# Performance work log

Measured on AMD Instinct MI355X. Metric: run time of the kernel, lower is better.

Reference implementation:

```python
import jax, jax.numpy as jnp
import numpy as np

DN = ('NHWC', 'HWIO', 'NHWC')
EPS = 1e-3  # Keras BatchNormalization default epsilon


def conv2d(x, w):
    return jax.lax.conv_general_dilated(x, w, (1, 1), 'SAME', dimension_numbers=DN)


def hard_sigmoid(x):
    # Keras ConvLSTM2D default recurrent_activation
    return jnp.clip(0.2 * x + 0.5, 0.0, 1.0)


def convlstm2d(x, Wx, Wh, b):
    """Keras ConvLSTM2D, return_sequences=True. x: (B,T,H,W,C).
    Wx: (3,3,C,4F) input kernel, Wh: (3,3,F,4F) recurrent kernel, b: (4F,).
    Gate order (Keras): i, f, c, o."""
    B, T, H, W, C = x.shape
    F = Wh.shape[2]
    # input-to-gate convs for all timesteps in one batched conv
    xg = conv2d(x.reshape(B * T, H, W, C), Wx) + b          # (B*T,H,W,4F)
    xg = xg.reshape(B, T, H, W, 4 * F).transpose(1, 0, 2, 3, 4)  # (T,B,H,W,4F)

    def step(carry, xg_t):
        h, c = carry
        g = xg_t + conv2d(h, Wh)                            # (B,H,W,4F)
        i, f, cc, o = jnp.split(g, 4, axis=-1)
        i = hard_sigmoid(i)
        f = hard_sigmoid(f)
        o = hard_sigmoid(o)
        c = f * c + i * jnp.tanh(cc)
        h = o * jnp.tanh(c)
        return (h, c), h

    h0 = jnp.zeros((B, H, W, F), x.dtype)
    (_, _), hs = jax.lax.scan(step, (h0, h0), xg)           # hs: (T,B,H,W,F)
    return hs.transpose(1, 0, 2, 3, 4)


def batchnorm(x, gamma, beta):
    # training-mode BN over all axes except channel (last)
    mu = x.mean(axis=(0, 1, 2, 3), keepdims=True)
    var = x.var(axis=(0, 1, 2, 3), keepdims=True)
    return gamma * (x - mu) * jax.lax.rsqrt(var + EPS) + beta


def setup_inputs() -> dict:
    key = jax.random.key(0)
    B, T, H, W, C = 4, 8, 16, 16, 256
    F = 256
    ks = jax.random.split(key, 10)
    s = 0.02
    inp = {
        'input_tensor': jax.random.normal(ks[0], (B, T, H, W, C), jnp.float32),
        'Wx1': jax.random.normal(ks[1], (3, 3, C, 4 * F), jnp.float32) * s,
        'Wh1': jax.random.normal(ks[2], (3, 3, F, 4 * F), jnp.float32) * s,
        'b1': jnp.zeros((4 * F,), jnp.float32),
        'g1': jnp.ones((F,), jnp.float32),
        'be1': jnp.zeros((F,), jnp.float32),
        'Wx2': jax.random.normal(ks[3], (3, 3, F, 4 * F), jnp.float32) * s,
        'Wh2': jax.random.normal(ks[4], (3, 3, F, 4 * F), jnp.float32) * s,
        'b2': jnp.zeros((4 * F,), jnp.float32),
        'g2': jnp.ones((F,), jnp.float32),
        'be2': jnp.zeros((F,), jnp.float32),
        'Wx3': jax.random.normal(ks[5], (3, 3, F, 4 * F), jnp.float32) * s,
        'Wh3': jax.random.normal(ks[6], (3, 3, F, 4 * F), jnp.float32) * s,
        'b3': jnp.zeros((4 * F,), jnp.float32),
        'g3': jnp.ones((F,), jnp.float32),
        'be3': jnp.zeros((F,), jnp.float32),
    }
    return inp


def reference(input_tensor, Wx1, Wh1, b1, g1, be1,
              Wx2, Wh2, b2, g2, be2,
              Wx3, Wh3, b3, g3, be3):
    x = batchnorm(convlstm2d(input_tensor, Wx1, Wh1, b1), g1, be1)
    x = batchnorm(convlstm2d(x, Wx2, Wh2, b2), g2, be2)
    x = batchnorm(convlstm2d(x, Wx3, Wh3, b3), g3, be3)
    return x
```

## Files before the change

kernel.cpp:

```cpp
#include <hip/hip_runtime.h>

#define HW      256
#define COUT    1024
#define TSTEPS  8
#define BN_EPS  1e-3f
#define KTOT    2304

typedef unsigned short u16;
typedef unsigned int   u32;
typedef __attribute__((ext_vector_type(8))) _Float16 v8h;
typedef __attribute__((ext_vector_type(4))) float v4f;

__device__ __forceinline__ u16 f2h(float x) {
    _Float16 h = (_Float16)x; return *(u16*)&h;
}
__device__ __forceinline__ float h2f(u16 u) {
    _Float16 h = *(_Float16*)&u; return (float)h;
}
__device__ __forceinline__ float hsig(float x) {
    return fminf(fmaxf(0.2f * x + 0.5f, 0.f), 1.f);
}

typedef __attribute__((address_space(1))) const unsigned int gas_u32;
typedef __attribute__((address_space(3))) unsigned int las_u32;
__device__ __forceinline__ void gl16(const void* g, void* l) {
    __builtin_amdgcn_global_load_lds((gas_u32*)g, (las_u32*)l, 16, 0, 0);
}

__global__ __launch_bounds__(256, 2) void conv_big_k(
    const u16* __restrict__ apad,
    const u16* __restrict__ wT,
    const float* __restrict__ bias,
    u16* __restrict__ out)
{
    constexpr int KQ = 36;
    __shared__ u16 lds[2 * 16384];

    const int bid = blockIdx.x;
    const int xcd = bid & 7, idx = bid >> 3;
    const int by = (xcd >> 1) * 2 + (idx & 1);
    const int bx = (xcd & 1) * 32 + (idx >> 1);
    const int m0 = bx * 128, n0 = by * 128;
    const int tid = threadIdx.x, lane = tid & 63, w = tid >> 6;
    const int wr = w >> 1, wc = w & 1;
    const int lr = lane >> 3;
    const int g  = (lane & 7) ^ lr;
    const int fr = lane & 15, kc = lane >> 4;

    const char* a_src[4];
    #pragma unroll
    for (int i = 0; i < 4; ++i) {
        int m = m0 + w * 32 + i * 8 + lr;
        int img = m >> 8, pix = m & 255, yy = pix >> 4, xx = pix & 15;
        a_src[i] = (const char*)apad + ((((long)img * 18 + yy) * 18 + xx) * 256 + g * 8) * 2;
    }
    const char* b_src[4];
    #pragma unroll
    for (int i = 0; i < 4; ++i) {
        int n = n0 + w * 32 + i * 8 + lr;
        b_src[i] = (const char*)wT + ((long)n * KTOT + g * 8) * 2;
    }

    int aro[4][2], bro[4][2];
    #pragma unroll
    for (int mi = 0; mi < 4; ++mi) {
        int rl = wr * 64 + mi * 16 + fr;
        #pragma unroll
        for (int ks = 0; ks < 2; ++ks)
            aro[mi][ks] = rl * 128 + ((((ks << 2) | kc) ^ (fr & 7)) << 4);
    }
    #pragma unroll
    for (int ni = 0; ni < 4; ++ni) {
        int nr = wc * 64 + ni * 16 + fr;
        #pragma unroll
        for (int ks = 0; ks < 2; ++ks)
            bro[ni][ks] = 16384 + nr * 128 + ((((ks << 2) | kc) ^ (fr & 7)) << 4);
    }

    v4f acc[4][4];
    #pragma unroll
    for (int mi = 0; mi < 4; ++mi)
        #pragma unroll
        for (int ni = 0; ni < 4; ++ni) acc[mi][ni] = (v4f)0.f;

#define STAGE_B(J) { int j_ = (J); int dxy = j_ >> 2, c64 = j_ & 3;           \
    int dy = (dxy * 11) >> 5; int dx = dxy - dy * 3;                          \
    int aoff = ((dy * 18 + dx) * 256 + c64 * 64) * 2; int boff = j_ * 128;    \
    char* base = (char*)lds + (j_ & 1) * 32768;                               \
    _Pragma("unroll") for (int i = 0; i < 4; ++i)                             \
        gl16(a_src[i] + aoff, base + (w * 32 + i * 8) * 128);                 \
    _Pragma("unroll") for (int i = 0; i < 4; ++i)                             \
        gl16(b_src[i] + boff, base + 16384 + (w * 32 + i * 8) * 128); }

#define COMPUTE_B(J) { const char* base = (const char*)lds + ((J) & 1) * 32768; \
    v8h af[4][2], bf[4][2];                                                   \
    _Pragma("unroll") for (int mi = 0; mi < 4; ++mi)                          \
        _Pragma("unroll") for (int ks = 0; ks < 2; ++ks)                      \
            af[mi][ks] = *(const v8h*)(base + aro[mi][ks]);                   \
    _Pragma("unroll") for (int ni = 0; ni < 4; ++ni)                          \
        _Pragma("unroll") for (int ks = 0; ks < 2; ++ks)                      \
            bf[ni][ks] = *(const v8h*)(base + bro[ni][ks]);                   \
    __builtin_amdgcn_s_setprio(1);                                            \
    _Pragma("unroll") for (int ks = 0; ks < 2; ++ks)                          \
    _Pragma("unroll") for (int mi = 0; mi < 4; ++mi)                          \
    _Pragma("unroll") for (int ni = 0; ni < 4; ++ni)                          \
        acc[mi][ni] = __builtin_amdgcn_mfma_f32_16x16x32_f16(af[mi][ks], bf[ni][ks], acc[mi][ni], 0, 0, 0); \
    __builtin_amdgcn_s_setprio(0); }

    STAGE_B(0);
    for (int kq = 0; kq < KQ - 1; ++kq) {
        asm volatile("s_waitcnt vmcnt(0)" ::: "memory");
        __builtin_amdgcn_s_barrier();
        __builtin_amdgcn_sched_barrier(0);
        STAGE_B(kq + 1);
        COMPUTE_B(kq);
    }
    asm volatile("s_waitcnt vmcnt(0)" ::: "memory");
    __builtin_amdgcn_s_barrier();
    __builtin_amdgcn_sched_barrier(0);
    COMPUTE_B(KQ - 1);
#undef STAGE_B
#undef COMPUTE_B

    #pragma unroll
    for (int mi = 0; mi < 4; ++mi) {
        #pragma unroll
        for (int ni = 0; ni < 4; ++ni) {
            int mrow = m0 + wr * 64 + mi * 16 + ((lane >> 4) << 2);
            int ncol = n0 + wc * 64 + ni * 16 + fr;
            float b0 = bias[(ncol & 3) * 256 + (ncol >> 2)];
            #pragma unroll
            for (int r = 0; r < 4; ++r)
                out[(long)(mrow + r) * COUT + ncol] = f2h(acc[mi][ni][r] + b0);
        }
    }
}

__global__ __launch_bounds__(256, 2) void rec_fused_k(
    const u16* __restrict__ ph_in,
    const u16* __restrict__ wT,
    const u16* __restrict__ xg,
    float* __restrict__ cbuf,
    float* __restrict__ hs,
    u16* __restrict__ ph_out,
    int t)
{
    constexpr int KQ = 36;
    __shared__ u16 lds[3 * 6144];

    const int bid = blockIdx.x;
    const int k8 = bid & 7, q = bid >> 3;
    const int by = k8 * 2 + (q >> 5), bx = q & 31;
    const int m0 = bx * 32, n0 = by * 64;
    const int tid = threadIdx.x, lane = tid & 63, wv = tid >> 6;
    const int lr = lane >> 3, g = (lane & 7) ^ lr;
    const int fr = lane & 15, kc = lane >> 4;

    const char* a_src;
    { int m = m0 + wv * 8 + lr;
      int img = m >> 8, pix = m & 255, yy = pix >> 4, xx = pix & 15;
      a_src = (const char*)ph_in + ((((long)img * 18 + yy) * 18 + xx) * 256 + g * 8) * 2; }
    const char* b_src[2];
    #pragma unroll
    for (int i = 0; i < 2; ++i) {
        int n = n0 + wv * 16 + i * 8 + lr;
        b_src[i] = (const char*)wT + ((long)n * KTOT + g * 8) * 2;
    }

    int aro[2][2], bro[2];
    #pragma unroll
    for (int mi = 0; mi < 2; ++mi)
        #pragma unroll
        for (int ks = 0; ks < 2; ++ks)
            aro[mi][ks] = (mi * 16 + fr) * 128 + ((((ks << 2) | kc) ^ (fr & 7)) << 4);
    #pragma unroll
    for (int ks = 0; ks < 2; ++ks)
        bro[ks] = 4096 + (wv * 16 + fr) * 128 + ((((ks << 2) | kc) ^ (fr & 7)) << 4);

    v4f acc0 = (v4f)0.f, acc1 = (v4f)0.f;

#define STAGE_R(J) { int j_ = (J); int dxy = j_ >> 2, c64 = j_ & 3;           \
    int dy = (dxy * 11) >> 5; int dx = dxy - dy * 3;                          \
    int aoff = ((dy * 18 + dx) * 256 + c64 * 64) * 2; int boff = j_ * 128;    \
    char* base = (char*)lds + (j_ % 3) * 12288;                               \
    gl16(a_src + aoff, base + (wv * 8) * 128);                                \
    gl16(b_src[0] + boff, base + 4096 + (wv * 16) * 128);                     \
    gl16(b_src[1] + boff, base + 4096 + (wv * 16 + 8) * 128); }

#define COMPUTE_R(J) { const char* base = (const char*)lds + ((J) % 3) * 12288; \
    v8h a00 = *(const v8h*)(base + aro[0][0]);                                \
    v8h a01 = *(const v8h*)(base + aro[0][1]);                                \
    v8h a10 = *(const v8h*)(base + aro[1][0]);                                \
    v8h a11 = *(const v8h*)(base + aro[1][1]);                                \
    v8h b0  = *(const v8h*)(base + bro[0]);                                   \
    v8h b1  = *(const v8h*)(base + bro[1]);                                   \
    __builtin_amdgcn_s_setprio(1);                                            \
    acc0 = __builtin_amdgcn_mfma_f32_16x16x32_f16(a00, b0, acc0, 0, 0, 0);    \
    acc1 = __builtin_amdgcn_mfma_f32_16x16x32_f16(a10, b0, acc1, 0, 0, 0);    \
    acc0 = __builtin_amdgcn_mfma_f32_16x16x32_f16(a01, b1, acc0, 0, 0, 0);    \
    acc1 = __builtin_amdgcn_mfma_f32_16x16x32_f16(a11, b1, acc1, 0, 0, 0);    \
    __builtin_amdgcn_s_setprio(0); }

    STAGE_R(0); STAGE_R(1);
    for (int kq = 0; kq < KQ - 2; ++kq) {
        asm volatile("s_waitcnt vmcnt(3)" ::: "memory");
        __builtin_amdgcn_s_barrier();
        __builtin_amdgcn_sched_barrier(0);
        STAGE_R(kq + 2);
        COMPUTE_R(kq);
    }
    asm volatile("s_waitcnt vmcnt(3)" ::: "memory");
    __builtin_amdgcn_s_barrier();
    __builtin_amdgcn_sched_barrier(0);
    COMPUTE_R(KQ - 2);
    asm volatile("s_waitcnt vmcnt(0)" ::: "memory");
    __builtin_amdgcn_s_barrier();
    __builtin_amdgcn_sched_barrier(0);
    COMPUTE_R(KQ - 1);
#undef STAGE_R
#undef COMPUTE_R

    v4f accA[2] = {acc0, acc1};
    const bool gl0 = lane & 1, gl1 = lane & 2;
    #pragma unroll
    for (int mi = 0; mi < 2; ++mi) {
        float V0 = accA[mi][0], V1 = accA[mi][1];
        float V2 = accA[mi][2], V3 = accA[mi][3];
        float x0 = __shfl_xor(V0, 1), x1 = __shfl_xor(V1, 1);
        float x2 = __shfl_xor(V2, 1), x3 = __shfl_xor(V3, 1);
        float a0 = gl0 ? x1 : V0;
        float a1 = gl0 ? V1 : x0;
        float a2 = gl0 ? x3 : V2;
        float a3 = gl0 ? V3 : x2;
        float s0 = __shfl_xor(a0, 2), s1 = __shfl_xor(a1, 2);
        float s2 = __shfl_xor(a2, 2), s3 = __shfl_xor(a3, 2);
        float Ti = gl1 ? s2 : a0;
        float Tf = gl1 ? s3 : a1;
        float Tc = gl1 ? a2 : s0;
        float To = gl1 ? a3 : s1;

        int row = m0 + mi * 16 + ((lane >> 4) << 2) + (lane & 3);
        int f4  = n0 + wv * 16 + (lane & 12);
        int img = row >> 8, pix = row & 255, fch = f4 >> 2;
        long xrow = ((long)(img * TSTEPS + t) * HW + pix);
        uint2 xb = *(const uint2*)&xg[xrow * COUT + f4];
        float pi = Ti + h2f((u16)(xb.x & 0xffff));
        float pf = Tf + h2f((u16)(xb.x >> 16));
        float pc = Tc + h2f((u16)(xb.y & 0xffff));
        float po = To + h2f((u16)(xb.y >> 16));
        long cidx = (long)row * 256 + fch;
        float c = hsig(pf) * cbuf[cidx] + hsig(pi) * tanhf(pc);
        float h = hsig(po) * tanhf(c);
        cbuf[cidx] = c;
        hs[xrow * 256 + fch] = h;
        int yy = pix >> 4, xx = pix & 15;
        ph_out[(((long)img * 18 + yy + 1) * 18 + xx + 1) * 256 + fch] = f2h(h);
    }
}

__global__ __launch_bounds__(256) void wprep_k(const float* __restrict__ w,
                                               u16* __restrict__ wT)
{
    int k0 = blockIdx.x * 32;
    int np = blockIdx.y * 256 + threadIdx.x;
    int n  = (np & 3) * 256 + (np >> 2);
    u32 pk[16];
    #pragma unroll
    for (int kk = 0; kk < 32; kk += 2) {
        float a = w[(long)(k0 + kk) * COUT + n];
        float b = w[(long)(k0 + kk + 1) * COUT + n];
        pk[kk >> 1] = (u32)f2h(a) | ((u32)f2h(b) << 16);
    }
    uint4* dst = (uint4*)&wT[(long)np * KTOT + k0];
    dst[0] = make_uint4(pk[0], pk[1], pk[2], pk[3]);
    dst[1] = make_uint4(pk[4], pk[5], pk[6], pk[7]);
    dst[2] = make_uint4(pk[8], pk[9], pk[10], pk[11]);
    dst[3] = make_uint4(pk[12], pk[13], pk[14], pk[15]);
}

__global__ __launch_bounds__(256) void convert_x_k(const float* __restrict__ x,
                                                   u16* __restrict__ padx)
{
    int q = blockIdx.x * 256 + threadIdx.x;
    int e0 = q * 4;
    int f = e0 & 255, pix = (e0 >> 8) & 255, img = e0 >> 16;
    float4 v = ((const float4*)x)[q];
    int yy = pix >> 4, xx = pix & 15;
    long o = (((long)img * 18 + yy + 1) * 18 + xx + 1) * 256 + f;
    u32 lo = (u32)f2h(v.x) | ((u32)f2h(v.y) << 16);
    u32 hi = (u32)f2h(v.z) | ((u32)f2h(v.w) << 16);
    *(uint2*)&padx[o] = make_uint2(lo, hi);
}

__global__ __launch_bounds__(256) void bn_stats1_k(
    const float* __restrict__ x, float* __restrict__ partial)
{
    const int tid = threadIdx.x;
    const int blk = blockIdx.x;
    float s = 0.f, s2 = 0.f;
    const long base = (long)blk * 16 * 256;
    #pragma unroll
    for (int gi = 0; gi < 16; ++gi) {
        float v = x[base + gi * 256 + tid];
        s += v; s2 += v * v;
    }
    partial[blk * 512 + tid]       = s;
    partial[blk * 512 + 256 + tid] = s2;
}

__global__ __launch_bounds__(256) void bn_stats2_k(
    const float* __restrict__ partial, const float* __restrict__ gamma,
    const float* __restrict__ beta, float* __restrict__ stats)
{
    const int f = threadIdx.x;
    float s = 0.f, s2 = 0.f;
    for (int b = 0; b < 512; ++b) {
        s  += partial[b * 512 + f];
        s2 += partial[b * 512 + 256 + f];
    }
    const float inv_n = 1.f / 8192.f;
    float mu  = s * inv_n;
    float var = s2 * inv_n - mu * mu;
    float sc  = gamma[f] * rsqrtf(var + BN_EPS);
    stats[f]       = sc;
    stats[256 + f] = beta[f] - mu * sc;
}

__global__ __launch_bounds__(256) void bn_apply_k(
    const float* __restrict__ x, const float* __restrict__ stats,
    u16* __restrict__ padx, float* __restrict__ out)
{
    const int q = blockIdx.x * 256 + threadIdx.x;
    const int e0 = q * 4;
    const int f = e0 & 255, pix = (e0 >> 8) & 255, img = e0 >> 16;
    float4 v  = ((const float4*)x)[q];
    float4 sc = *(const float4*)(stats + f);
    float4 sh = *(const float4*)(stats + 256 + f);
    v.x = v.x * sc.x + sh.x;
    v.y = v.y * sc.y + sh.y;
    v.z = v.z * sc.z + sh.z;
    v.w = v.w * sc.w + sh.w;
    if (out) ((float4*)out)[q] = v;
    if (padx) {
        int yy = pix >> 4, xx = pix & 15;
        long o = (((long)img * 18 + yy + 1) * 18 + xx + 1) * 256 + f;
        u32 lo = (u32)f2h(v.x) | ((u32)f2h(v.y) << 16);
        u32 hi = (u32)f2h(v.z) | ((u32)f2h(v.w) << 16);
        *(uint2*)&padx[o] = make_uint2(lo, hi);
    }
}

extern "C" void kernel_launch(void* const* d_in, const int* in_sizes, int n_in,
                              void* d_out, int out_size, void* d_ws, size_t ws_size,
                              hipStream_t stream)
{
    const float* x0    = (const float*)d_in[0];
    const float* Wx[3] = {(const float*)d_in[1], (const float*)d_in[6],  (const float*)d_in[11]};
    const float* Wh[3] = {(const float*)d_in[2], (const float*)d_in[7],  (const float*)d_in[12]};
    const float* bb[3] = {(const float*)d_in[3], (const float*)d_in[8],  (const float*)d_in[13]};
    const float* gg[3] = {(const float*)d_in[4], (const float*)d_in[9],  (const float*)d_in[14]};
    const float* be[3] = {(const float*)d_in[5], (const float*)d_in[10], (const float*)d_in[15]};

    float* ws    = (float*)d_ws;
    u16*  xg     = (u16*)ws;
    float* cbuf  = ws   + 4194304;
    float* hs    = cbuf + 262144;
    float* part  = hs   + 2097152;
    float* stats = part + 262144;
    u16*  pad_x  = (u16*)(stats + 512);
    u16*  pad_h  = pad_x + 2654208;
    u16*  wTx    = pad_h + 663552;
    u16*  wTh    = wTx   + 2359296;
    const long PHN = 331776;

    hipMemsetAsync(pad_x, 0, 2654208 * sizeof(u16), stream);
    hipLaunchKernelGGL(convert_x_k, dim3(2048), dim3(256), 0, stream, x0, pad_x);

    for (int l = 0; l < 3; ++l) {
        hipLaunchKernelGGL(wprep_k, dim3(72, 4), dim3(256), 0, stream, Wx[l], wTx);
        hipLaunchKernelGGL(wprep_k, dim3(72, 4), dim3(256), 0, stream, Wh[l], wTh);

        hipLaunchKernelGGL(conv_big_k, dim3(512), dim3(256), 0, stream,
            pad_x, wTx, bb[l], xg);

        hipMemsetAsync(pad_h, 0, 2 * PHN * sizeof(u16), stream);
        hipMemsetAsync(cbuf, 0, 262144 * sizeof(float), stream);

        for (int t = 0; t < TSTEPS; ++t) {
            hipLaunchKernelGGL(rec_fused_k, dim3(512), dim3(256), 0, stream,
                pad_h + (t & 1) * PHN, wTh, xg, cbuf, hs,
                pad_h + ((t & 1) ^ 1) * PHN, t);
        }

        hipLaunchKernelGGL(bn_stats1_k, dim3(512), dim3(256), 0, stream, hs, part);
        hipLaunchKernelGGL(bn_stats2_k, dim3(1), dim3(256), 0, stream, part, gg[l], be[l], stats);
        hipLaunchKernelGGL(bn_apply_k, dim3(2048), dim3(256), 0, stream, hs, stats,
            (l < 2) ? pad_x : (u16*)nullptr, (l == 2) ? (float*)d_out : (float*)nullptr);
    }
}
```

Before: 587.2 us.

## Restructure recurrent GEMM with fragment-ordered weights and skip zero-state first step

The recurrent kernel now uses 64x64 tiles with 256 blocks. Weights are pre-packed into MFMA fragment order by a new prep kernel and loaded straight into registers, double-buffered, instead of being staged through LDS. Timestep 0, where h and c are zero, is replaced by a gate-only kernel, which removes one recurrent GEMM per layer. The padded h buffer is zeroed once rather than per layer, and BN stats use fewer, larger partial blocks. In exchange, 256 blocks on this GPU gives lower occupancy and less latency hiding, and the register-held B fragments raise register pressure.

```diff
diff --git a/kernel.cpp b/kernel.cpp
--- a/kernel.cpp
+++ b/kernel.cpp
@@ -136,94 +136,104 @@
     }
 }
 
-__global__ __launch_bounds__(256, 2) void rec_fused_k(
+__global__ __launch_bounds__(256) void rec_fused_k(
     const u16* __restrict__ ph_in,
-    const u16* __restrict__ wT,
+    const u16* __restrict__ wTf,
     const u16* __restrict__ xg,
     float* __restrict__ cbuf,
     float* __restrict__ hs,
     u16* __restrict__ ph_out,
     int t)
 {
-    constexpr int KQ = 36;
-    __shared__ u16 lds[3 * 6144];
+    __shared__ u16 lds[3 * 4096];
 
     const int bid = blockIdx.x;
-    const int k8 = bid & 7, q = bid >> 3;
-    const int by = k8 * 2 + (q >> 5), bx = q & 31;
-    const int m0 = bx * 32, n0 = by * 64;
-    const int tid = threadIdx.x, lane = tid & 63, wv = tid >> 6;
+    const int by = (bid & 7) * 2 + ((bid >> 3) & 1);
+    const int bx = bid >> 4;
+    const int m0 = bx * 64, n0 = by * 64;
+    const int tid = threadIdx.x, lane = tid & 63, w = tid >> 6;
     const int lr = lane >> 3, g = (lane & 7) ^ lr;
     const int fr = lane & 15, kc = lane >> 4;
 
-    const char* a_src;
-    { int m = m0 + wv * 8 + lr;
-      int img = m >> 8, pix = m & 255, yy = pix >> 4, xx = pix & 15;
-      a_src = (const char*)ph_in + ((((long)img * 18 + yy) * 18 + xx) * 256 + g * 8) * 2; }
-    const char* b_src[2];
+    const char* a_src[2];
     #pragma unroll
     for (int i = 0; i < 2; ++i) {
-        int n = n0 + wv * 16 + i * 8 + lr;
-        b_src[i] = (const char*)wT + ((long)n * KTOT + g * 8) * 2;
-    }
-
-    int aro[2][2], bro[2];
-    #pragma unroll
-    for (int mi = 0; mi < 2; ++mi)
+        int m = m0 + w * 16 + i * 8 + lr;
+        int img = m >> 8, pix = m & 255, yy = pix >> 4, xx = pix & 15;
+        a_src[i] = (const char*)ph_in + ((((long)img * 18 + yy) * 18 + xx) * 256 + g * 8) * 2;
+    }
+    const char* b_base = (const char*)wTf + ((long)(by * 4 + w) * 72) * 1024 + lane * 16;
+
+    int aro[4][2];
+    #pragma unroll
+    for (int mi = 0; mi < 4; ++mi)
         #pragma unroll
         for (int ks = 0; ks < 2; ++ks)
             aro[mi][ks] = (mi * 16 + fr) * 128 + ((((ks << 2) | kc) ^ (fr & 7)) << 4);
-    #pragma unroll
-    for (int ks = 0; ks < 2; ++ks)
-        bro[ks] = 4096 + (wv * 16 + fr) * 128 + ((((ks << 2) | kc) ^ (fr & 7)) << 4);
-
-    v4f acc0 = (v4f)0.f, acc1 = (v4f)0.f;
-
-#define STAGE_R(J) { int j_ = (J); int dxy = j_ >> 2, c64 = j_ & 3;           \
+
+    v4f acc0 = (v4f)0.f, acc1 = (v4f)0.f, acc2 = (v4f)0.f, acc3 = (v4f)0.f;
+    v8h b0x, b0y, b1x, b1y;
+
+#define STAGE_A(J) { int j_ = (J); int dxy = j_ >> 2, c64 = j_ & 3;           \
     int dy = (dxy * 11) >> 5; int dx = dxy - dy * 3;                          \
-    int aoff = ((dy * 18 + dx) * 256 + c64 * 64) * 2; int boff = j_ * 128;    \
-    char* base = (char*)lds + (j_ % 3) * 12288;                               \
-    gl16(a_src + aoff, base + (wv * 8) * 128);                                \
-    gl16(b_src[0] + boff, base + 4096 + (wv * 16) * 128);                     \
-    gl16(b_src[1] + boff, base + 4096 + (wv * 16 + 8) * 128); }
-
-#define COMPUTE_R(J) { const char* base = (const char*)lds + ((J) % 3) * 12288; \
-    v8h a00 = *(const v8h*)(base + aro[0][0]);                                \
-    v8h a01 = *(const v8h*)(base + aro[0][1]);                                \
-    v8h a10 = *(const v8h*)(base + aro[1][0]);                                \
-    v8h a11 = *(const v8h*)(base + aro[1][1]);                                \
-    v8h b0  = *(const v8h*)(base + bro[0]);                                   \
-    v8h b1  = *(const v8h*)(base + bro[1]);                                   \
+    int aoff = ((dy * 18 + dx) * 256 + c64 * 64) * 2;                         \
+    char* dst = (char*)lds + (j_ % 3) * 8192 + (w * 16) * 128;                \
+    gl16(a_src[0] + aoff, dst); gl16(a_src[1] + aoff, dst + 1024); }
+
+#define LDB(J, RX, RY) { RX = *(const v8h*)(b_base + (2 * (J)) * 1024);       \
+                         RY = *(const v8h*)(b_base + (2 * (J) + 1) * 1024); }
+
+#define COMPUTE(J, RX, RY) { const char* base = (const char*)lds + ((J) % 3) * 8192; \
+    v8h af0 = *(const v8h*)(base + aro[0][0]);                                \
+    v8h af1 = *(const v8h*)(base + aro[1][0]);                                \
+    v8h af2 = *(const v8h*)(base + aro[2][0]);                                \
+    v8h af3 = *(const v8h*)(base + aro[3][0]);                                \
+    v8h ag0 = *(const v8h*)(base + aro[0][1]);                                \
+    v8h ag1 = *(const v8h*)(base + aro[1][1]);                                \
+    v8h ag2 = *(const v8h*)(base + aro[2][1]);                                \
+    v8h ag3 = *(const v8h*)(base + aro[3][1]);                                \
     __builtin_amdgcn_s_setprio(1);                                            \
-    acc0 = __builtin_amdgcn_mfma_f32_16x16x32_f16(a00, b0, acc0, 0, 0, 0);    \
-    acc1 = __builtin_amdgcn_mfma_f32_16x16x32_f16(a10, b0, acc1, 0, 0, 0);    \
-    acc0 = __builtin_amdgcn_mfma_f32_16x16x32_f16(a01, b1, acc0, 0, 0, 0);    \
-    acc1 = __builtin_amdgcn_mfma_f32_16x16x32_f16(a11, b1, acc1, 0, 0, 0);    \
+    acc0 = __builtin_amdgcn_mfma_f32_16x16x32_f16(af0, RX, acc0, 0, 0, 0);    \
+    acc1 = __builtin_amdgcn_mfma_f32_16x16x32_f16(af1, RX, acc1, 0, 0, 0);    \
+    acc2 = __builtin_amdgcn_mfma_f32_16x16x32_f16(af2, RX, acc2, 0, 0, 0);    \
+    acc3 = __builtin_amdgcn_mfma_f32_16x16x32_f16(af3, RX, acc3, 0, 0, 0);    \
+    acc0 = __builtin_amdgcn_mfma_f32_16x16x32_f16(ag0, RY, acc0, 0, 0, 0);    \
+    acc1 = __builtin_amdgcn_mfma_f32_16x16x32_f16(ag1, RY, acc1, 0, 0, 0);    \
+    acc2 = __builtin_amdgcn_mfma_f32_16x16x32_f16(ag2, RY, acc2, 0, 0, 0);    \
+    acc3 = __builtin_amdgcn_mfma_f32_16x16x32_f16(ag3, RY, acc3, 0, 0, 0);    \
     __builtin_amdgcn_s_setprio(0); }
 
-    STAGE_R(0); STAGE_R(1);
-    for (int kq = 0; kq < KQ - 2; ++kq) {
-        asm volatile("s_waitcnt vmcnt(3)" ::: "memory");
+    STAGE_A(0); LDB(0, b0x, b0y); STAGE_A(1);
+    for (int j = 0; j < 17; ++j) {
+        int kq = 2 * j;
+        asm volatile("s_waitcnt vmcnt(2)" ::: "memory");
         __builtin_amdgcn_s_barrier();
         __builtin_amdgcn_sched_barrier(0);
-        STAGE_R(kq + 2);
-        COMPUTE_R(kq);
-    }
-    asm volatile("s_waitcnt vmcnt(3)" ::: "memory");
+        LDB(kq + 1, b1x, b1y); STAGE_A(kq + 2);
+        COMPUTE(kq, b0x, b0y);
+        asm volatile("s_waitcnt vmcnt(2)" ::: "memory");
+        __builtin_amdgcn_s_barrier();
+        __builtin_amdgcn_sched_barrier(0);
+        LDB(kq + 2, b0x, b0y); STAGE_A(kq + 3);
+        COMPUTE(kq + 1, b1x, b1y);
+    }
+    asm volatile("s_waitcnt vmcnt(2)" ::: "memory");
     __builtin_amdgcn_s_barrier();
     __builtin_amdgcn_sched_barrier(0);
-    COMPUTE_R(KQ - 2);
+    LDB(35, b1x, b1y);
+    COMPUTE(34, b0x, b0y);
     asm volatile("s_waitcnt vmcnt(0)" ::: "memory");
     __builtin_amdgcn_s_barrier();
     __builtin_amdgcn_sched_barrier(0);
-    COMPUTE_R(KQ - 1);
-#undef STAGE_R
-#undef COMPUTE_R
-
-    v4f accA[2] = {acc0, acc1};
+    COMPUTE(35, b1x, b1y);
+#undef STAGE_A
+#undef LDB
+#undef COMPUTE
+
+    v4f accA[4] = {acc0, acc1, acc2, acc3};
     const bool gl0 = lane & 1, gl1 = lane & 2;
     #pragma unroll
-    for (int mi = 0; mi < 2; ++mi) {
+    for (int mi = 0; mi < 4; ++mi) {
         float V0 = accA[mi][0], V1 = accA[mi][1];
         float V2 = accA[mi][2], V3 = accA[mi][3];
         float x0 = __shfl_xor(V0, 1), x1 = __shfl_xor(V1, 1);
@@ -240,7 +250,7 @@
         float To = gl1 ? a3 : s1;
 
         int row = m0 + mi * 16 + ((lane >> 4) << 2) + (lane & 3);
-        int f4  = n0 + wv * 16 + (lane & 12);
+        int f4  = n0 + w * 16 + (lane & 12);
         int img = row >> 8, pix = row & 255, fch = f4 >> 2;
         long xrow = ((long)(img * TSTEPS + t) * HW + pix);
         uint2 xb = *(const uint2*)&xg[xrow * COUT + f4];
@@ -258,6 +268,26 @@
     }
 }
 
+__global__ __launch_bounds__(256) void gates0_k(
+    const u16* __restrict__ xg, float* __restrict__ cbuf,
+    float* __restrict__ hs, u16* __restrict__ ph_out)
+{
+    int idx = blockIdx.x * 256 + threadIdx.x;
+    int fch = idx & 255, row = idx >> 8;
+    int img = row >> 8, pix = row & 255;
+    long xrow = (long)(img * TSTEPS) * HW + pix;
+    uint2 xb = *(const uint2*)&xg[xrow * COUT + fch * 4];
+    float pi = h2f((u16)(xb.x & 0xffff));
+    float pc = h2f((u16)(xb.y & 0xffff));
+    float po = h2f((u16)(xb.y >> 16));
+    float c = hsig(pi) * tanhf(pc);
+    float h = hsig(po) * tanhf(c);
+    cbuf[(long)row * 256 + fch] = c;
+    hs[xrow * 256 + fch] = h;
+    int yy = pix >> 4, xx = pix & 15;
+    ph_out[(((long)img * 18 + yy + 1) * 18 + xx + 1) * 256 + fch] = f2h(h);
+}
+
 __global__ __launch_bounds__(256) void wprep_k(const float* __restrict__ w,
                                                u16* __restrict__ wT)
 {
@@ -276,6 +306,26 @@
     dst[1] = make_uint4(pk[4], pk[5], pk[6], pk[7]);
     dst[2] = make_uint4(pk[8], pk[9], pk[10], pk[11]);
     dst[3] = make_uint4(pk[12], pk[13], pk[14], pk[15]);
+}
+
+__global__ __launch_bounds__(256) void wprep_frag_k(const float* __restrict__ w,
+                                                    u16* __restrict__ wTf)
+{
+    int kq = blockIdx.x;
+    int nf = blockIdx.y * 4 + (threadIdx.x >> 6);
+    int l  = threadIdx.x & 63;
+    int np = nf * 16 + (l & 15);
+    int n  = (np & 3) * 256 + (np >> 2);
+    int k0 = kq * 32 + (l >> 4) * 8;
+    u32 pk[4];
+    #pragma unroll
+    for (int e = 0; e < 8; e += 2) {
+        float a = w[(long)(k0 + e) * COUT + n];
+        float b = w[(long)(k0 + e + 1) * COUT + n];
+        pk[e >> 1] = (u32)f2h(a) | ((u32)f2h(b) << 16);
+    }
+    *(uint4*)&wTf[((long)(nf * 72) + kq) * 512 + l * 8] =
+        make_uint4(pk[0], pk[1], pk[2], pk[3]);
 }
 
 __global__ __launch_bounds__(256) void convert_x_k(const float* __restrict__ x,
@@ -298,9 +348,9 @@
     const int tid = threadIdx.x;
     const int blk = blockIdx.x;
     float s = 0.f, s2 = 0.f;
-    const long base = (long)blk * 16 * 256;
-    #pragma unroll
-    for (int gi = 0; gi < 16; ++gi) {
+    const long base = (long)blk * 128 * 256;
+    #pragma unroll 8
+    for (int gi = 0; gi < 128; ++gi) {
         float v = x[base + gi * 256 + tid];
         s += v; s2 += v * v;
     }
@@ -314,7 +364,8 @@
 {
     const int f = threadIdx.x;
     float s = 0.f, s2 = 0.f;
-    for (int b = 0; b < 512; ++b) {
+    #pragma unroll 8
+    for (int b = 0; b < 64; ++b) {
         s  += partial[b * 512 + f];
         s2 += partial[b * 512 + 256 + f];
     }
@@ -370,29 +421,30 @@
     u16*  pad_x  = (u16*)(stats + 512);
     u16*  pad_h  = pad_x + 2654208;
     u16*  wTx    = pad_h + 663552;
-    u16*  wTh    = wTx   + 2359296;
+    u16*  wTf    = wTx   + 2359296;
     const long PHN = 331776;
 
     hipMemsetAsync(pad_x, 0, 2654208 * sizeof(u16), stream);
+    hipMemsetAsync(pad_h, 0, 2 * PHN * sizeof(u16), stream);
     hipLaunchKernelGGL(convert_x_k, dim3(2048), dim3(256), 0, stream, x0, pad_x);
 
     for (int l = 0; l < 3; ++l) {
         hipLaunchKernelGGL(wprep_k, dim3(72, 4), dim3(256), 0, stream, Wx[l], wTx);
-        hipLaunchKernelGGL(wprep_k, dim3(72, 4), dim3(256), 0, stream, Wh[l], wTh);
+        hipLaunchKernelGGL(wprep_frag_k, dim3(72, 16), dim3(256), 0, stream, Wh[l], wTf);
 
         hipLaunchKernelGGL(conv_big_k, dim3(512), dim3(256), 0, stream,
             pad_x, wTx, bb[l], xg);
 
-        hipMemsetAsync(pad_h, 0, 2 * PHN * sizeof(u16), stream);
-        hipMemsetAsync(cbuf, 0, 262144 * sizeof(float), stream);
-
-        for (int t = 0; t < TSTEPS; ++t) {
-            hipLaunchKernelGGL(rec_fused_k, dim3(512), dim3(256), 0, stream,
-                pad_h + (t & 1) * PHN, wTh, xg, cbuf, hs,
+        hipLaunchKernelGGL(gates0_k, dim3(1024), dim3(256), 0, stream,
+            xg, cbuf, hs, pad_h + PHN);
+
+        for (int t = 1; t < TSTEPS; ++t) {
+            hipLaunchKernelGGL(rec_fused_k, dim3(256), dim3(256), 0, stream,
+                pad_h + (t & 1) * PHN, wTf, xg, cbuf, hs,
                 pad_h + ((t & 1) ^ 1) * PHN, t);
         }
 
-        hipLaunchKernelGGL(bn_stats1_k, dim3(512), dim3(256), 0, stream, hs, part);
+        hipLaunchKernelGGL(bn_stats1_k, dim3(64), dim3(256), 0, stream, hs, part);
         hipLaunchKernelGGL(bn_stats2_k, dim3(1), dim3(256), 0, stream, part, gg[l], be[l], stats);
         hipLaunchKernelGGL(bn_apply_k, dim3(2048), dim3(256), 0, stream, hs, stats,
             (l < 2) ? pad_x : (u16*)nullptr, (l == 2) ? (float*)d_out : (float*)nullptr);
```

Measured after the change: 554.2 us. -5.6%, faster.
